# Kernel tuning notes

Hardware: AMD Instinct MI355X
Metric: run time of the kernel (lower is better)

## Reference

```python
import jax, jax.numpy as jnp
import numpy as np

N, E, EL = 50000, 150000, 300000   # atoms, bonds(=line-graph nodes), line-graph edges
FN, FE, FX = 128, 128, 64          # atom, bond, angle feature dims (encode_dim)
H, D = 4, 64                        # num_heads, per-head hidden
SLOPE = 0.01                        # torch leaky_relu default


def _leaky(x):
    return jnp.where(x >= 0, x, SLOPE * x)


def _seg_softmax(logits, seg, n):
    # softmax over edges grouped by destination (DGL edge_softmax). logits [E, H]
    m = jax.ops.segment_max(logits, seg, num_segments=n)
    ex = jnp.exp(logits - m[seg])
    s = jax.ops.segment_sum(ex, seg, num_segments=n)
    return ex / s[seg]


def _seg_mean(x, seg, n):
    # mean of incoming edge feats per dst node; empty segments -> 0 (DGL behavior)
    s = jax.ops.segment_sum(x, seg, num_segments=n)
    c = jax.ops.segment_sum(jnp.ones((x.shape[0], 1), x.dtype), seg, num_segments=n)
    return s / jnp.maximum(c, 1.0)


def setup_inputs() -> dict:
    key = jax.random.key(0)
    ks = iter(jax.random.split(key, 40))
    nrm = lambda shape, sc=0.1: jax.random.normal(next(ks), shape, jnp.float32) * sc
    z = lambda n: jnp.zeros((n,), jnp.float32)
    inp = {
        'nfeats': nrm((N, FN), 1.0),
        'efeats': nrm((E, FE), 1.0),
        'xfeats': nrm((EL, FX), 1.0),
        # EGAT layer (atom graph)
        'e_Wni': nrm((H * D, FN)), 'e_Wnj': nrm((H * D, FN)), 'e_Wfij': nrm((H * D, FE)),
        'e_Wnode': nrm((H * D, FN + FE)), 'e_bnode': z(H * D),
        'e_attn': nrm((H, D)), 'e_bias': z(H * D),
        # Path_Complex line-graph branch
        'lg_Wni': nrm((H * D, D)), 'lg_Wnj': nrm((H * D, D)), 'lg_Wfij': nrm((H * D, FX)),
        'lg_Wnode': nrm((H * D, D + FX)), 'lg_bnode': z(H * D),
        'lg_attn': nrm((H, D)), 'lg_bias': z(H * D),
        # Path_Complex graph branch
        'g_Wni': nrm((H * D, D)), 'g_Wnj': nrm((H * D, D)), 'g_Wfij': nrm((H * D, D)),
        'g_Wnode': nrm((H * D, D + D)), 'g_bnode': z(H * D),
        'g_attn': nrm((H, D)), 'g_bias': z(H * D),
        # graph / line-graph connectivity
        'src': jax.random.randint(next(ks), (E,), 0, N, jnp.int32),
        'dst': jax.random.randint(next(ks), (E,), 0, N, jnp.int32),
        'lsrc': jax.random.randint(next(ks), (EL,), 0, E, jnp.int32),
        'ldst': jax.random.randint(next(ks), (EL,), 0, E, jnp.int32),
    }
    return inp


def _forward(nfeats, efeats, xfeats,
             e_Wni, e_Wnj, e_Wfij, e_Wnode, e_bnode, e_attn, e_bias,
             lg_Wni, lg_Wnj, lg_Wfij, lg_Wnode, lg_bnode, lg_attn, lg_bias,
             g_Wni, g_Wnj, g_Wfij, g_Wnode, g_bnode, g_attn, g_bias,
             src, dst, lsrc, ldst):
    # ---- EGAT layer on atom graph ----
    fo = _leaky((nfeats @ e_Wni.T)[src] + (nfeats @ e_Wnj.T)[dst] + efeats @ e_Wfij.T + e_bias)
    fov = fo.reshape(E, H, D)
    e_att = _seg_softmax((fov * e_attn[None]).sum(-1), dst, N)      # [E, H]
    agg = _seg_mean(efeats, dst, N)                                   # [N, FE]
    h = (jnp.concatenate([nfeats, agg], 1) @ e_Wnode.T + e_bnode).reshape(N, H, D)
    h_node = _leaky(jax.ops.segment_sum(h[src] * e_att[:, :, None], dst, num_segments=N)).sum(1)
    f_edge = fov.sum(1)                                               # [E, D]

    # ---- Path_Complex layer: line-graph (bond->angle) branch ----
    lgf = _leaky((f_edge @ lg_Wni.T)[lsrc] + (f_edge @ lg_Wnj.T)[ldst] + xfeats @ lg_Wfij.T + lg_bias)
    lgv = lgf.reshape(EL, H, D)
    a_lg = _seg_softmax((lgv * lg_attn[None]).sum(-1), ldst, E)      # [EL, H]
    aggx = _seg_mean(xfeats, ldst, E)                                 # [E, FX]
    m1 = (jnp.concatenate([f_edge, aggx], 1) @ lg_Wnode.T + lg_bnode).reshape(E, H, D)
    lg_h = _leaky(jax.ops.segment_sum(m1[lsrc] * a_lg[:, :, None], ldst, num_segments=E)).sum(1)

    # ---- Path_Complex layer: graph (atom->bond) branch ----
    gf = _leaky((h_node @ g_Wni.T)[src] + (h_node @ g_Wnj.T)[dst] + f_edge @ g_Wfij.T + g_bias)
    gv = gf.reshape(E, H, D)
    a_g = _seg_softmax((gv * g_attn[None]).sum(-1), dst, N)          # [E, H] -> l_graph ndata 'a'
    node_edge = h_node[src] + h_node[dst]
    m2 = (jnp.concatenate([node_edge, f_edge], 1) @ g_Wnode.T + g_bnode).reshape(E, H, D)
    # u_mul_v on line graph: message = h_out[lsrc] * a[ldst]
    g_h = _leaky(jax.ops.segment_sum(m2[lsrc] * a_g[ldst][:, :, None], ldst, num_segments=E)).sum(1)

    return g_h + lg_h                                                 # [E, D] updated bond feats


def reference(nfeats, efeats, xfeats,
              e_Wni, e_Wnj, e_Wfij, e_Wnode, e_bnode, e_attn, e_bias,
              lg_Wni, lg_Wnj, lg_Wfij, lg_Wnode, lg_bnode, lg_attn, lg_bias,
              g_Wni, g_Wnj, g_Wfij, g_Wnode, g_bnode, g_attn, g_bias,
              src, dst, lsrc, ldst):
    return _forward(nfeats, efeats, xfeats,
                    e_Wni, e_Wnj, e_Wfij, e_Wnode, e_bnode, e_attn, e_bias,
                    lg_Wni, lg_Wnj, lg_Wfij, lg_Wnode, lg_bnode, lg_attn, lg_bias,
                    g_Wni, g_Wnj, g_Wfij, g_Wnode, g_bnode, g_attn, g_bias,
                    src, dst, lsrc, ldst)
```

## Files before the change

### kernel.cpp

```cpp
#include <hip/hip_runtime.h>
#include <hip/hip_bf16.h>
#include <math.h>

typedef __hip_bfloat16 bf16;
typedef short bf16x8 __attribute__((ext_vector_type(8)));
typedef short s16x4 __attribute__((ext_vector_type(4)));
typedef float f32x4 __attribute__((ext_vector_type(4)));

__device__ __forceinline__ float b2f(bf16 x) { return __bfloat162float(x); }
__device__ __forceinline__ bf16  f2b(float x) { return __float2bfloat16(x); }
__device__ __forceinline__ float leaky(float x) { return x >= 0.0f ? x : 0.01f * x; }
__device__ __forceinline__ float sb2f(short s) {
  return __uint_as_float(((unsigned)(unsigned short)s) << 16);
}
__device__ __forceinline__ short f2bs(float x) {
  unsigned u = __float_as_uint(x);
  u += 0x7FFFu + ((u >> 16) & 1u);
  return (short)(u >> 16);
}
__device__ __forceinline__ float ldF(const void* p, size_t i, int f) {
  return f ? ((const float*)p)[i] : b2f(((const bf16*)p)[i]);
}
__device__ __forceinline__ bf16x8 ldA8(const char* row, int k, int f) {
  if (!f) return *(const bf16x8*)(row + (size_t)k * 2);
  const float4* p = (const float4*)(row + (size_t)k * 4);
  float4 a = p[0], b = p[1];
  bf16x8 r;
  r[0] = f2bs(a.x); r[1] = f2bs(a.y); r[2] = f2bs(a.z); r[3] = f2bs(a.w);
  r[4] = f2bs(b.x); r[5] = f2bs(b.y); r[6] = f2bs(b.z); r[7] = f2bs(b.w);
  return r;
}
__device__ __forceinline__ bf16x8 ldA8sum(const bf16* base, int K0, int s, int t, int k) {
  bf16x8 u = *(const bf16x8*)(base + (size_t)s * K0 + k);
  bf16x8 v = *(const bf16x8*)(base + (size_t)t * K0 + k);
  bf16x8 r;
#pragma unroll
  for (int j = 0; j < 8; ++j) r[j] = f2bs(sb2f(u[j]) + sb2f(v[j]));
  return r;
}

__global__ void k_detect(const unsigned* __restrict__ w, int* __restrict__ flag) {
  __shared__ int cnt[256];
  unsigned x = w[threadIdx.x];
  unsigned ex = (x >> 7) & 0xFFu;
  cnt[threadIdx.x] = (ex >= 96u && ex <= 144u) ? 1 : 0;
  __syncthreads();
  for (int s = 128; s > 0; s >>= 1) {
    if (threadIdx.x < s) cnt[threadIdx.x] += cnt[threadIdx.x + s];
    __syncthreads();
  }
  if (threadIdx.x == 0) *flag = (cnt[0] < 128) ? 1 : 0;
}

struct WArgs { const void* src[21]; int beg[22]; int len[21]; };
__global__ void k_cvt_all(WArgs wa, bf16* __restrict__ dst, int total,
                          const int* __restrict__ flagp) {
  int f = *flagp;
  for (int i = blockIdx.x * 256 + threadIdx.x; i < total; i += gridDim.x * 256) {
    int t = 0;
    while (t < 20 && i >= wa.beg[t + 1]) ++t;
    int loc = i - wa.beg[t];
    bf16 v = f2b(0.0f);
    if (loc < wa.len[t])
      v = f ? f2b(((const float*)wa.src[t])[loc]) : ((const bf16*)wa.src[t])[loc];
    dst[i] = v;
  }
}

__global__ void k_cvt3(const float* __restrict__ a, bf16* __restrict__ da, size_t na,
                       const float* __restrict__ b, bf16* __restrict__ db, size_t nb,
                       const float* __restrict__ c, bf16* __restrict__ dc, size_t nc,
                       const int* __restrict__ flagp) {
  if (!*flagp) return;
  size_t tot = (na + nb + nc) >> 2;
  for (size_t i = (size_t)blockIdx.x * 256 + threadIdx.x; i < tot;
       i += (size_t)gridDim.x * 256) {
    size_t j = i << 2;
    const float* s; bf16* d; size_t loc;
    if (j < na)           { s = a; d = da; loc = j; }
    else if (j < na + nb) { s = b; d = db; loc = j - na; }
    else                  { s = c; d = dc; loc = j - na - nb; }
    float4 v = *(const float4*)(s + loc);
    s16x4 o; o[0] = f2bs(v.x); o[1] = f2bs(v.y); o[2] = f2bs(v.z); o[3] = f2bs(v.w);
    *(s16x4*)(d + loc) = o;
  }
}

__global__ void k_izero(int* __restrict__ p, int n) {
  int i = blockIdx.x * 256 + threadIdx.x;
  for (; i < n; i += gridDim.x * 256) p[i] = 0;
}

__global__ void k_hist(const int* __restrict__ seg, int* __restrict__ deg, int n) {
  int i = blockIdx.x * 256 + threadIdx.x;
  if (i < n) atomicAdd(&deg[seg[i]], 1);
}

__global__ __launch_bounds__(256)
void k_scan_local(const int* __restrict__ deg, int* __restrict__ rp,
                  int* __restrict__ bsum, int n) {
  __shared__ int sh[256];
  int tid = threadIdx.x;
  int base = blockIdx.x * 4096 + tid * 16;
  int v[16]; int s = 0;
#pragma unroll
  for (int j = 0; j < 16; ++j) { v[j] = (base + j < n) ? deg[base + j] : 0; s += v[j]; }
  sh[tid] = s;
  __syncthreads();
  for (int o = 1; o < 256; o <<= 1) {
    int t = (tid >= o) ? sh[tid - o] : 0;
    __syncthreads();
    sh[tid] += t;
    __syncthreads();
  }
  int run = sh[tid] - s;
#pragma unroll
  for (int j = 0; j < 16; ++j) {
    run += v[j];
    if (base + j < n) rp[base + j + 1] = run;
  }
  if (tid == 255) bsum[blockIdx.x] = sh[255];
  if (blockIdx.x == 0 && tid == 0) rp[0] = 0;
}
__global__ __launch_bounds__(256)
void k_scan_bsum(int* __restrict__ bsum, int nb) {
  __shared__ int sh[256];
  __shared__ int carry;
  int tid = threadIdx.x;
  if (tid == 0) carry = 0;
  __syncthreads();
  for (int base = 0; base < nb; base += 256) {
    int i = base + tid;
    int v = (i < nb) ? bsum[i] : 0;
    sh[tid] = v;
    __syncthreads();
    for (int o = 1; o < 256; o <<= 1) {
      int t = (tid >= o) ? sh[tid - o] : 0;
      __syncthreads();
      sh[tid] += t;
      __syncthreads();
    }
    if (i < nb) bsum[i] = carry + sh[tid] - v;
    int tot = sh[255];
    __syncthreads();
    if (tid == 0) carry += tot;
    __syncthreads();
  }
}
__global__ __launch_bounds__(256)
void k_scan_add(int* __restrict__ rp, const int* __restrict__ bsum, int n) {
  int b = blockIdx.x + 1;
  int ofs = bsum[b];
  int base = b * 4096 + threadIdx.x * 16;
#pragma unroll
  for (int j = 0; j < 16; ++j) {
    int idx = base + j + 1;
    if (idx <= n) rp[idx] += ofs;
  }
}

__global__ void k_slot(const int* __restrict__ seg, const int* __restrict__ rp,
                       int* __restrict__ cur, int* __restrict__ eid,
                       const int* __restrict__ aux, int* __restrict__ auxval,
                       int* __restrict__ pos, int n) {
  int i = blockIdx.x * 256 + threadIdx.x;
  if (i >= n) return;
  int t = seg[i];
  int p = atomicAdd(&cur[t], 1);
  int j = rp[t] + p;
  eid[j] = i;
  if (auxval) auxval[j] = aux[i];
  if (pos) pos[i] = j;
}

__global__ void k_gmean(const void* __restrict__ X, const void* __restrict__ Xc, int mode,
                        const int* __restrict__ rp, const int* __restrict__ eid,
                        bf16* __restrict__ out, int n, int width,
                        const int* __restrict__ flagp) {
  int f = (mode == 2) ? *flagp : mode;
  if (Xc && f) { X = Xc; f = 0; }
  int d = threadIdx.x;
  int row = blockIdx.x * blockDim.y + threadIdx.y;
  if (row >= n) return;
  int b = rp[row], e = rp[row + 1];
  float s = 0.0f;
  for (int j = b; j < e; ++j) s += ldF(X, (size_t)eid[j] * width + d, f);
  out[(size_t)row * width + d] = f2b(s / fmaxf((float)(e - b), 1.0f));
}

__global__ __launch_bounds__(256)
void k_mgemm(const void* __restrict__ A0, const void* __restrict__ A0c, int m0mode, int K0,
             const void* __restrict__ A1, int m1mode, int Ktot,
             const bf16* __restrict__ W, int whs, const bf16* __restrict__ bias,
             bf16* __restrict__ C, int cs, int M,
             const int* __restrict__ gs, const int* __restrict__ gd,
             const int* __restrict__ flagp) {
  int tid = threadIdx.x;
  int w = tid >> 6, lane = tid & 63, l15 = lane & 15, q = lane >> 4;
  int h = blockIdx.y;
  int fl = *flagp;
  int f0 = (m0mode == 2) ? fl : m0mode;
  if (A0c && f0) { A0 = A0c; f0 = 0; }
  int f1 = (m1mode == 2) ? fl : m1mode;
  const bf16* Wh = W + (size_t)h * whs;
  int colofs = h * 64;
  int m0 = blockIdx.x * 64 + w * 16;
  int mA = m0 + l15; if (mA > M - 1) mA = M - 1;
  int sA = 0, tA = 0;
  const char* rowA0 = nullptr;
  if (gs) { sA = gs[mA]; tA = gd[mA]; }
  else rowA0 = (const char*)A0 + (size_t)mA * K0 * (f0 ? 4 : 2);
  const char* rowA1 = A1 ? (const char*)A1 + (size_t)mA * (Ktot - K0) * (f1 ? 4 : 2) : nullptr;

  f32x4 acc[4] = {{0,0,0,0},{0,0,0,0},{0,0,0,0},{0,0,0,0}};
  for (int k = q * 8; k < Ktot; k += 32) {
    bf16x8 a;
    if (k < K0) a = gs ? ldA8sum((const bf16*)A0, K0, sA, tA, k) : ldA8(rowA0, k, f0);
    else        a = ldA8(rowA1, k - K0, f1);
    const bf16* wb = Wh + (size_t)l15 * Ktot + k;
#pragma unroll
    for (int t = 0; t < 4; ++t)
      acc[t] = __builtin_amdgcn_mfma_f32_16x16x32_bf16(
          a, *(const bf16x8*)(wb + (size_t)(t * 16) * Ktot), acc[t], 0, 0, 0);
  }
#pragma unroll
  for (int t = 0; t < 4; ++t) {
    int col = t * 16 + l15;
    float bv = bias ? b2f(bias[colofs + col]) : 0.0f;
#pragma unroll
    for (int r = 0; r < 4; ++r) {
      int m = m0 + q * 4 + r;
      if (m < M) C[(size_t)m * cs + colofs + col] = f2b(acc[t][r] + bv);
    }
  }
}

__global__ __launch_bounds__(256)
void k_mgemm2(const void* __restrict__ A, const void* __restrict__ Ac, int mode, int K,
              const bf16* __restrict__ W1, const bf16* __restrict__ W2, int whs,
              bf16* __restrict__ C1, bf16* __restrict__ C2, int cs, int M,
              const int* __restrict__ flagp) {
  int tid = threadIdx.x;
  int w = tid >> 6, lane = tid & 63, l15 = lane & 15, q = lane >> 4;
  int h = blockIdx.y;
  int f = (mode == 2) ? *flagp : mode;
  if (Ac && f) { A = Ac; f = 0; }
  const bf16* W1h = W1 + (size_t)h * whs;
  const bf16* W2h = W2 + (size_t)h * whs;
  int colofs = h * 64;
  int m0 = blockIdx.x * 64 + w * 16;
  int mA = m0 + l15; if (mA > M - 1) mA = M - 1;
  const char* rowA = (const char*)A + (size_t)mA * K * (f ? 4 : 2);

  f32x4 a1[4] = {{0,0,0,0},{0,0,0,0},{0,0,0,0},{0,0,0,0}};
  f32x4 a2[4] = {{0,0,0,0},{0,0,0,0},{0,0,0,0},{0,0,0,0}};
  for (int k = q * 8; k < K; k += 32) {
    bf16x8 a = ldA8(rowA, k, f);
    const bf16* w1 = W1h + (size_t)l15 * K + k;
    const bf16* w2 = W2h + (size_t)l15 * K + k;
#pragma unroll
    for (int t = 0; t < 4; ++t) {
      a1[t] = __builtin_amdgcn_mfma_f32_16x16x32_bf16(
          a, *(const bf16x8*)(w1 + (size_t)(t * 16) * K), a1[t], 0, 0, 0);
      a2[t] = __builtin_amdgcn_mfma_f32_16x16x32_bf16(
          a, *(const bf16x8*)(w2 + (size_t)(t * 16) * K), a2[t], 0, 0, 0);
    }
  }
#pragma unroll
  for (int r = 0; r < 4; ++r) {
    int m = m0 + q * 4 + r;
    if (m < M) {
      s16x4 o1, o2;
#pragma unroll
      for (int t = 0; t < 4; ++t) { o1[t] = f2bs(a1[t][r]); o2[t] = f2bs(a2[t][r]); }
      *(s16x4*)(C1 + (size_t)m * cs + colofs + l15 * 4) = o1;
      *(s16x4*)(C2 + (size_t)m * cs + colofs + l15 * 4) = o2;
    }
  }
}

template<int NK>
__global__ __launch_bounds__(256)
void k_mcomb4(const void* __restrict__ A, const void* __restrict__ Ac, int mode,
              const bf16* __restrict__ W, int whs,
              const bf16* __restrict__ bias, const bf16* __restrict__ attn,
              const bf16* __restrict__ G1, const bf16* __restrict__ G2, int gstr,
              const int* __restrict__ gi, const int* __restrict__ gj,
              const int* __restrict__ posw,
              float* __restrict__ lg4, bf16* __restrict__ fout,
              int M, const int* __restrict__ flagp) {
  constexpr int K = NK * 32;
  int tid = threadIdx.x;
  int w = tid >> 6, lane = tid & 63, l15 = lane & 15, q = lane >> 4;
  int f = (mode == 2) ? *flagp : mode;
  if (Ac && f) { A = Ac; f = 0; }
  int m0 = blockIdx.x * 64 + w * 16;
  int mA = m0 + l15; if (mA > M - 1) mA = M - 1;
  const char* rowA = (const char*)A + (size_t)mA * K * (f ? 4 : 2);
  bf16x8 af[NK];
#pragma unroll
  for (int i = 0; i < NK; ++i) af[i] = ldA8(rowA, q * 8 + 32 * i, f);
  int sIdx[4], dIdx[4], pIdx[4]; bool okr[4];
#pragma unroll
  for (int r = 0; r < 4; ++r) {
    int m = m0 + q * 4 + r;
    okr[r] = m < M; int mc = okr[r] ? m : M - 1;
    sIdx[r] = gi[mc]; dIdx[r] = gj[mc];
    pIdx[r] = posw ? posw[mc] : mc;
  }
  s16x4 gv1[4][4], gv2[4][4];
#pragma unroll
  for (int r = 0; r < 4; ++r) {
    const s16x4* p1 = (const s16x4*)(G1 + (size_t)sIdx[r] * gstr) + l15;
    const s16x4* p2 = (const s16x4*)(G2 + (size_t)dIdx[r] * gstr) + l15;
#pragma unroll
    for (int h = 0; h < 4; ++h) { gv1[r][h] = p1[h * 16]; gv2[r][h] = p2[h * 16]; }
  }
  f32x4 fs[4] = {{0,0,0,0},{0,0,0,0},{0,0,0,0},{0,0,0,0}};
#pragma unroll
  for (int h = 0; h < 4; ++h) {
    const bf16* Wh = W + (size_t)h * whs;
    f32x4 acc[4] = {{0,0,0,0},{0,0,0,0},{0,0,0,0},{0,0,0,0}};
#pragma unroll
    for (int i = 0; i < NK; ++i) {
      const bf16* wb = Wh + (size_t)l15 * K + q * 8 + 32 * i;
#pragma unroll
      for (int t = 0; t < 4; ++t)
        acc[t] = __builtin_amdgcn_mfma_f32_16x16x32_bf16(
            af[i], *(const bf16x8*)(wb + (size_t)(t * 16) * K), acc[t], 0, 0, 0);
    }
    float bv[4], av[4];
#pragma unroll
    for (int t = 0; t < 4; ++t) {
      bv[t] = b2f(bias[h * 64 + t * 16 + l15]);
      av[t] = b2f(attn[h * 64 + t * 16 + l15]);
    }
    float part[4];
#pragma unroll
    for (int r = 0; r < 4; ++r) {
      float p = 0.0f;
#pragma unroll
      for (int t = 0; t < 4; ++t) {
        float v = acc[t][r] + bv[t] + sb2f(gv1[r][h][t]) + sb2f(gv2[r][h][t]);
        v = leaky(v);
        p += v * av[t];
        fs[t][r] += v;
      }
      part[r] = p;
    }
#pragma unroll
    for (int o = 1; o < 16; o <<= 1)
#pragma unroll
      for (int r = 0; r < 4; ++r) part[r] += __shfl_xor(part[r], o, 64);
    if (l15 == 0) {
#pragma unroll
      for (int r = 0; r < 4; ++r)
        if (okr[r]) lg4[(size_t)pIdx[r] * 4 + h] = part[r];
    }
  }
  if (fout) {
#pragma unroll
    for (int t = 0; t < 4; ++t) {
      int col = t * 16 + l15;
#pragma unroll
      for (int r = 0; r < 4; ++r)
        if (okr[r]) fout[(size_t)(m0 + q * 4 + r) * 64 + col] = f2b(fs[t][r]);
    }
  }
}

__global__ __launch_bounds__(256)
void k_mcomb(const void* __restrict__ A, const void* __restrict__ Ac, int mode, int K,
             const bf16* __restrict__ W, const bf16* __restrict__ bias,
             const bf16* __restrict__ attn,
             const bf16* __restrict__ G1, const bf16* __restrict__ G2, int gstr,
             const int* __restrict__ gi, const int* __restrict__ gj,
             const int* __restrict__ posw,
             float* __restrict__ lg, int M, const int* __restrict__ flagp) {
  int tid = threadIdx.x;
  int w = tid >> 6, lane = tid & 63, l15 = lane & 15, q = lane >> 4;
  int f = (mode == 2) ? *flagp : mode;
  if (Ac && f) { A = Ac; f = 0; }
  int m0 = blockIdx.x * 64 + w * 16;
  int mA = m0 + l15; if (mA > M - 1) mA = M - 1;
  const char* rowA = (const char*)A + (size_t)mA * K * (f ? 4 : 2);
  int mcs[4], pIdx[4]; bool okr[4];
#pragma unroll
  for (int r = 0; r < 4; ++r) {
    int m = m0 + q * 4 + r;
    okr[r] = m < M; mcs[r] = okr[r] ? m : M - 1;
    pIdx[r] = posw ? posw[mcs[r]] : mcs[r];
  }
  s16x4 gv1[4], gv2[4];
#pragma unroll
  for (int r = 0; r < 4; ++r) {
    gv1[r] = ((const s16x4*)(G1 + (size_t)gi[mcs[r]] * gstr))[l15];
    gv2[r] = ((const s16x4*)(G2 + (size_t)gj[mcs[r]] * gstr))[l15];
  }
  f32x4 acc[4] = {{0,0,0,0},{0,0,0,0},{0,0,0,0},{0,0,0,0}};
  for (int k = q * 8; k < K; k += 32) {
    bf16x8 a = ldA8(rowA, k, f);
    const bf16* wb = W + (size_t)l15 * K + k;
#pragma unroll
    for (int t = 0; t < 4; ++t)
      acc[t] = __builtin_amdgcn_mfma_f32_16x16x32_bf16(
          a, *(const bf16x8*)(wb + (size_t)(t * 16) * K), acc[t], 0, 0, 0);
  }
  float attv[4], bsv[4];
#pragma unroll
  for (int t = 0; t < 4; ++t) { attv[t] = b2f(attn[t*16+l15]); bsv[t] = b2f(bias[t*16+l15]); }
  float part[4];
#pragma unroll
  for (int r = 0; r < 4; ++r) {
    float p = 0.0f;
#pragma unroll
    for (int t = 0; t < 4; ++t) {
      float v = acc[t][r] + bsv[t] + sb2f(gv1[r][t]) + sb2f(gv2[r][t]);
      p += leaky(v) * attv[t];
    }
    part[r] = p;
  }
#pragma unroll
  for (int o = 1; o < 16; o <<= 1)
#pragma unroll
    for (int r = 0; r < 4; ++r) part[r] += __shfl_xor(part[r], o, 64);
  if (l15 == 0) {
#pragma unroll
    for (int r = 0; r < 4; ++r)
      if (okr[r]) lg[pIdx[r]] = part[r];
  }
}

__global__ __launch_bounds__(256)
void k_smax4_csr(float* __restrict__ lg, const int* __restrict__ rp, int n) {
  int tid = blockIdx.x * 256 + threadIdx.x;
  int row = tid >> 2, h = tid & 3;
  if (row >= n) return;
  int b = rp[row], e = rp[row + 1];
  float m = -INFINITY;
  for (int j = b; j < e; ++j) m = fmaxf(m, lg[(size_t)j * 4 + h]);
  float s = 0.0f;
  for (int j = b; j < e; ++j) {
    float ex = expf(lg[(size_t)j * 4 + h] - m);
    lg[(size_t)j * 4 + h] = ex;
    s += ex;
  }
  float inv = 1.0f / s;
  for (int j = b; j < e; ++j) lg[(size_t)j * 4 + h] *= inv;
}
__global__ __launch_bounds__(256)
void k_smax4_eid(float* __restrict__ lg, const int* __restrict__ rp,
                 const int* __restrict__ eid, int n) {
  int tid = blockIdx.x * 256 + threadIdx.x;
  int row = tid >> 2, h = tid & 3;
  if (row >= n) return;
  int b = rp[row], e = rp[row + 1];
  float m = -INFINITY;
  for (int j = b; j < e; ++j) m = fmaxf(m, lg[(size_t)eid[j] * 4 + h]);
  float s = 0.0f;
  for (int j = b; j < e; ++j) {
    float ex = expf(lg[(size_t)eid[j] * 4 + h] - m);
    lg[(size_t)eid[j] * 4 + h] = ex;
    s += ex;
  }
  float inv = 1.0f / s;
  for (int j = b; j < e; ++j) lg[(size_t)eid[j] * 4 + h] *= inv;
}
__global__ __launch_bounds__(256)
void k_smax1_csr(float* __restrict__ lg, const int* __restrict__ rp, int n) {
  int row = blockIdx.x * 256 + threadIdx.x;
  if (row >= n) return;
  int b = rp[row], e = rp[row + 1];
  float m = -INFINITY;
  for (int j = b; j < e; ++j) m = fmaxf(m, lg[j]);
  float s = 0.0f;
  for (int j = b; j < e; ++j) { float ex = expf(lg[j] - m); lg[j] = ex; s += ex; }
  float inv = 1.0f / s;
  for (int j = b; j < e; ++j) lg[j] *= inv;
}

__global__ __launch_bounds__(256)
void k_ghnode(const bf16* __restrict__ H, const float* __restrict__ lg4c,
              const int* __restrict__ rp, const int* __restrict__ srcv,
              bf16* __restrict__ hnode, int N) {
  int d = threadIdx.x, h = threadIdx.y;
  int n = blockIdx.x;
  int b = rp[n], e = rp[n + 1];
  float s = 0.0f;
  for (int j = b; j < e; ++j)
    s += b2f(H[(size_t)srcv[j] * 256 + h * 64 + d]) * lg4c[(size_t)j * 4 + h];
  float v = leaky(s);
  __shared__ float sh[4][64];
  if (h > 0) sh[h][d] = v;
  __syncthreads();
  if (h == 0)
    hnode[(size_t)n * 64 + d] = f2b(v + sh[1][d] + sh[2][d] + sh[3][d]);
}

__global__ void k_gout2(const bf16* __restrict__ M1, const float* __restrict__ lgE,
                        const int* __restrict__ rp, const int* __restrict__ lsv,
                        float* __restrict__ out, int E, int first) {
  int d = threadIdx.x;
  int t = blockIdx.x * 4 + threadIdx.y;
  if (t >= E) return;
  int b = rp[t], e = rp[t + 1];
  float s = 0.0f;
  for (int j = b; j < e; ++j)
    s += b2f(M1[(size_t)lsv[j] * 64 + d]) * lgE[j];
  float val = leaky(s);
  if (first) out[(size_t)t * 64 + d] = val;
  else       out[(size_t)t * 64 + d] += val;
}

__global__ void k_gout3(const bf16* __restrict__ M2, const float* __restrict__ lg4n,
                        const int* __restrict__ rp, const int* __restrict__ lsv,
                        float* __restrict__ out, int E, int h) {
  int d = threadIdx.x;
  int t = blockIdx.x * 4 + threadIdx.y;
  if (t >= E) return;
  int b = rp[t], e = rp[t + 1];
  float s = 0.0f;
  for (int j = b; j < e; ++j) s += b2f(M2[(size_t)lsv[j] * 64 + d]);
  float a = lg4n[(size_t)t * 4 + h];
  out[(size_t)t * 64 + d] += leaky(a * s);
}

__global__ void k_addpair(const bf16* __restrict__ hn, const int* __restrict__ src,
                          const int* __restrict__ dst, bf16* __restrict__ ne, int E) {
  int d = threadIdx.x;
  int e = blockIdx.x * 4 + threadIdx.y;
  if (e >= E) return;
  ne[(size_t)e * 64 + d] =
      f2b(b2f(hn[(size_t)src[e] * 64 + d]) + b2f(hn[(size_t)dst[e] * 64 + d]));
}

__global__ void k_cast(void* __restrict__ out, const float* __restrict__ a, size_t n,
                       const int* __restrict__ flagp) {
  int f = *flagp;
  size_t i = (size_t)blockIdx.x * blockDim.x + threadIdx.x;
  size_t st = (size_t)gridDim.x * blockDim.x;
  for (; i < n; i += st) {
    if (f) ((float*)out)[i] = a[i];
    else   ((bf16*)out)[i] = f2b(a[i]);
  }
}

extern "C" void kernel_launch(void* const* d_in, const int* in_sizes, int n_in,
                              void* d_out, int out_size, void* d_ws, size_t ws_size,
                              hipStream_t stream) {
  const int* src  = (const int*)d_in[24];
  const int* dst  = (const int*)d_in[25];
  const int* lsrc = (const int*)d_in[26];
  const int* ldst = (const int*)d_in[27];

  const int N  = in_sizes[0] / 128;
  const int E  = in_sizes[24];
  const int EL = in_sizes[26];
  (void)n_in; (void)out_size; (void)ws_size;

  char* base = (char*)d_ws;
  size_t off = 0;
  auto alloc = [&](size_t bytes) -> char* {
    char* p = base + off;
    off = (off + bytes + 255) & ~(size_t)255;
    return p;
  };
  int* flag = (int*)alloc(256);
  size_t wofs[28]; size_t wtot = 0;
  for (int i = 3; i <= 23; ++i) { wofs[i] = wtot; wtot += (size_t)((in_sizes[i] + 127) & ~127); }
  bf16* WA = (bf16*)alloc(wtot * 2);

  int*   tmpi  = (int*)alloc((size_t)2 * E * 4);
  int*   rpN   = (int*)alloc((size_t)(N + 1) * 4);
  int*   eidN  = (int*)alloc((size_t)E * 4);
  int*   srcv  = (int*)alloc((size_t)E * 4);
  int*   posN  = (int*)alloc((size_t)E * 4);
  int*   rpE   = (int*)alloc((size_t)(E + 1) * 4);
  int*   eidEL = (int*)alloc((size_t)EL * 4);
  int*   lsv   = (int*)alloc((size_t)EL * 4);
  int*   posE  = (int*)alloc((size_t)EL * 4);
  int*   bsum  = (int*)alloc(((size_t)((E > N ? E : N) + 4095) / 4096 + 8) * 4);
  bf16*  fedge = (bf16*)alloc((size_t)E * 64 * 2);
  bf16*  hnode = (bf16*)alloc((size_t)N * 64 * 2);
  float* outacc= (float*)alloc((size_t)E * 64 * 4);
  bf16*  aggB  = (bf16*)alloc((size_t)E * 64 * 2);
  bf16*  SA    = (bf16*)alloc((size_t)N * 256 * 2 > (size_t)E * 64 * 2
                              ? (size_t)N * 256 * 2 : (size_t)E * 64 * 2);
  bf16*  SB    = (bf16*)alloc((size_t)N * 256 * 2 > (size_t)E * 64 * 2
                              ? (size_t)N * 256 * 2 : (size_t)E * 64 * 2);
  float* logE4 = (float*)alloc((size_t)E * 4 * 4);
  float* logh  = (float*)alloc((size_t)EL * 4);
  bf16*  nb    = (bf16*)alloc((size_t)N * 128 * 2);

  bf16* eb = (bf16*)outacc;
  bf16* xb = (bf16*)d_out;

  dim3 blk(256);
  const unsigned tN = (N + 63) / 64, tEg = (E + 63) / 64, tELg = (EL + 63) / 64;
  const unsigned gE4 = (E + 3) / 4, gN4 = (N + 3) / 4;
  const unsigned cE = (E + 255) / 256, cEL = (EL + 255) / 256;
  const int nbN = (N + 4095) / 4096, nbE = (E + 4095) / 4096;

  k_detect<<<dim3(1), blk, 0, stream>>>((const unsigned*)d_in[0], flag);
  WArgs wa;
  for (int i = 3; i <= 23; ++i) {
    wa.src[i - 3] = d_in[i];
    wa.beg[i - 3] = (int)wofs[i];
    wa.len[i - 3] = in_sizes[i];
  }
  wa.beg[21] = (int)wtot;
  k_cvt_all<<<dim3(512), blk, 0, stream>>>(wa, WA, (int)wtot, flag);
  k_cvt3<<<dim3(2048), blk, 0, stream>>>(
      (const float*)d_in[0], nb, (size_t)N * 128,
      (const float*)d_in[1], eb, (size_t)E * 128,
      (const float*)d_in[2], xb, (size_t)EL * 64, flag);

  int* deg = tmpi; int* cur = tmpi + E;
  k_izero<<<dim3(1024), blk, 0, stream>>>(tmpi, 2 * E);
  k_hist<<<dim3(cE), blk, 0, stream>>>(dst, deg, E);
  k_scan_local<<<dim3(nbN), blk, 0, stream>>>(deg, rpN, bsum, N);
  k_scan_bsum<<<dim3(1), blk, 0, stream>>>(bsum, nbN);
  if (nbN > 1) k_scan_add<<<dim3(nbN - 1), blk, 0, stream>>>(rpN, bsum, N);
  k_slot<<<dim3(cE), blk, 0, stream>>>(dst, rpN, cur, eidN, src, srcv, posN, E);
  k_izero<<<dim3(1024), blk, 0, stream>>>(tmpi, 2 * E);
  k_hist<<<dim3(cEL), blk, 0, stream>>>(ldst, deg, EL);
  k_scan_local<<<dim3(nbE), blk, 0, stream>>>(deg, rpE, bsum, E);
  k_scan_bsum<<<dim3(1), blk, 0, stream>>>(bsum, nbE);
  if (nbE > 1) k_scan_add<<<dim3(nbE - 1), blk, 0, stream>>>(rpE, bsum, E);
  k_slot<<<dim3(cEL), blk, 0, stream>>>(ldst, rpE, cur, eidEL, lsrc, lsv, posE, EL);

  k_gmean<<<dim3((N + 1) / 2), dim3(128, 2), 0, stream>>>(d_in[1], eb, 2, rpN, eidN,
                                                          aggB, N, 128, flag);
  k_mgemm2<<<dim3(tN, 4), blk, 0, stream>>>(d_in[0], nb, 2, 128, WA + wofs[3], WA + wofs[4],
                                            8192, SA, SB, 256, N, flag);
  k_mcomb4<4><<<dim3(tEg), blk, 0, stream>>>(d_in[1], eb, 2, WA + wofs[5], 8192,
      WA + wofs[9], WA + wofs[8], SA, SB, 256, src, dst, posN, logE4, fedge, E, flag);
  k_smax4_csr<<<dim3((N * 4 + 255) / 256), blk, 0, stream>>>(logE4, rpN, N);
  k_mgemm<<<dim3(tN, 4), blk, 0, stream>>>(d_in[0], nb, 2, 128, aggB, 0, 256,
      WA + wofs[6], 16384, WA + wofs[7], SA, 256, N, nullptr, nullptr, flag);
  k_ghnode<<<dim3(N), dim3(64, 4), 0, stream>>>(SA, logE4, rpN, srcv, hnode, N);

  k_gmean<<<dim3(gE4), dim3(64, 4), 0, stream>>>(d_in[2], xb, 2, rpE, eidEL, aggB, E, 64, flag);
  for (int h = 0; h < 4; ++h) {
    k_mgemm2<<<dim3(tEg), blk, 0, stream>>>(fedge, nullptr, 0, 64,
        WA + wofs[10] + h * 4096, WA + wofs[11] + h * 4096, 0, SA, SB, 64, E, flag);
    k_mcomb<<<dim3(tELg), blk, 0, stream>>>(d_in[2], xb, 2, 64,
        WA + wofs[12] + h * 4096, WA + wofs[16] + h * 64, WA + wofs[15] + h * 64,
        SA, SB, 64, lsrc, ldst, posE, logh, EL, flag);
    k_smax1_csr<<<dim3((E + 255) / 256), blk, 0, stream>>>(logh, rpE, E);
    k_mgemm<<<dim3(tEg, 1), blk, 0, stream>>>(fedge, nullptr, 0, 64, aggB, 0, 128,
        WA + wofs[13] + (size_t)h * 8192, 0, WA + wofs[14] + h * 64,
        SA, 64, E, nullptr, nullptr, flag);
    k_gout2<<<dim3(gE4), dim3(64, 4), 0, stream>>>(SA, logh, rpE, lsv,
                                                   outacc, E, h == 0 ? 1 : 0);
  }

  k_mgemm2<<<dim3(tN, 4), blk, 0, stream>>>(hnode, nullptr, 0, 64, WA + wofs[17], WA + wofs[18],
                                            4096, SA, SB, 256, N, flag);
  k_mcomb4<2><<<dim3(tEg), blk, 0, stream>>>(fedge, nullptr, 0, WA + wofs[19], 4096,
      WA + wofs[23], WA + wofs[22], SA, SB, 256, src, dst, nullptr, logE4, nullptr, E, flag);
  k_smax4_eid<<<dim3((N * 4 + 255) / 256), blk, 0, stream>>>(logE4, rpN, eidN, N);
  k_addpair<<<dim3(gE4), dim3(64, 4), 0, stream>>>(hnode, src, dst, aggB, E);
  for (int h = 0; h < 4; ++h) {
    k_mgemm<<<dim3(tEg, 1), blk, 0, stream>>>(aggB, nullptr, 0, 64, fedge, 0, 128,
        WA + wofs[20] + (size_t)h * 8192, 0, WA + wofs[21] + h * 64,
        SB, 64, E, nullptr, nullptr, flag);
    k_gout3<<<dim3(gE4), dim3(64, 4), 0, stream>>>(SB, logE4, rpE, lsv,
                                                   outacc, E, h);
  }

  k_cast<<<dim3(2048), blk, 0, stream>>>(d_out, outacc, (size_t)E * 64, flag);
}
```

Before: 1.804 ms.

## Batch line-graph attention logits two heads per pass with swizzled gather layout

Replaces the per-head line-graph logit pipeline (projection GEMM, combine, single-head softmax) with two passes that each handle two heads. The combine kernel reuses loaded A fragments across both heads and writes into a 4-wide logit buffer, followed by one multi-head CSR softmax. Projection outputs are stored in a swizzled layout so each lane gathers 8 or 16 contiguous bf16 values per endpoint instead of several 4-element chunks. It also drops the efeats bf16 pre-conversion and shrinks buffers, which adds more register pressure and a larger logit buffer.

Result: no change. 1.838 ms (+1.9%).

```diff
diff --git a/kernel.cpp b/kernel.cpp
--- a/kernel.cpp
+++ b/kernel.cpp
@@ -28,14 +28,6 @@
   bf16x8 r;
   r[0] = f2bs(a.x); r[1] = f2bs(a.y); r[2] = f2bs(a.z); r[3] = f2bs(a.w);
   r[4] = f2bs(b.x); r[5] = f2bs(b.y); r[6] = f2bs(b.z); r[7] = f2bs(b.w);
-  return r;
-}
-__device__ __forceinline__ bf16x8 ldA8sum(const bf16* base, int K0, int s, int t, int k) {
-  bf16x8 u = *(const bf16x8*)(base + (size_t)s * K0 + k);
-  bf16x8 v = *(const bf16x8*)(base + (size_t)t * K0 + k);
-  bf16x8 r;
-#pragma unroll
-  for (int j = 0; j < 8; ++j) r[j] = f2bs(sb2f(u[j]) + sb2f(v[j]));
   return r;
 }
 
@@ -67,19 +59,17 @@
   }
 }
 
-__global__ void k_cvt3(const float* __restrict__ a, bf16* __restrict__ da, size_t na,
-                       const float* __restrict__ b, bf16* __restrict__ db, size_t nb,
+__global__ void k_cvt2(const float* __restrict__ a, bf16* __restrict__ da, size_t na,
                        const float* __restrict__ c, bf16* __restrict__ dc, size_t nc,
                        const int* __restrict__ flagp) {
   if (!*flagp) return;
-  size_t tot = (na + nb + nc) >> 2;
+  size_t tot = (na + nc) >> 2;
   for (size_t i = (size_t)blockIdx.x * 256 + threadIdx.x; i < tot;
        i += (size_t)gridDim.x * 256) {
     size_t j = i << 2;
     const float* s; bf16* d; size_t loc;
-    if (j < na)           { s = a; d = da; loc = j; }
-    else if (j < na + nb) { s = b; d = db; loc = j - na; }
-    else                  { s = c; d = dc; loc = j - na - nb; }
+    if (j < na) { s = a; d = da; loc = j; }
+    else        { s = c; d = dc; loc = j - na; }
     float4 v = *(const float4*)(s + loc);
     s16x4 o; o[0] = f2bs(v.x); o[1] = f2bs(v.y); o[2] = f2bs(v.z); o[3] = f2bs(v.w);
     *(s16x4*)(d + loc) = o;
@@ -161,7 +151,7 @@
 
 __global__ void k_slot(const int* __restrict__ seg, const int* __restrict__ rp,
                        int* __restrict__ cur, int* __restrict__ eid,
-                       const int* __restrict__ aux, int* __restrict__ auxval,
+                       const int* __restrict__ aux1, int* __restrict__ av1,
                        int* __restrict__ pos, int n) {
   int i = blockIdx.x * 256 + threadIdx.x;
   if (i >= n) return;
@@ -169,7 +159,7 @@
   int p = atomicAdd(&cur[t], 1);
   int j = rp[t] + p;
   eid[j] = i;
-  if (auxval) auxval[j] = aux[i];
+  if (av1) av1[j] = aux1[i];
   if (pos) pos[i] = j;
 }
 
@@ -193,7 +183,6 @@
              const void* __restrict__ A1, int m1mode, int Ktot,
              const bf16* __restrict__ W, int whs, const bf16* __restrict__ bias,
              bf16* __restrict__ C, int cs, int M,
-             const int* __restrict__ gs, const int* __restrict__ gd,
              const int* __restrict__ flagp) {
   int tid = threadIdx.x;
   int w = tid >> 6, lane = tid & 63, l15 = lane & 15, q = lane >> 4;
@@ -206,16 +195,13 @@
   int colofs = h * 64;
   int m0 = blockIdx.x * 64 + w * 16;
   int mA = m0 + l15; if (mA > M - 1) mA = M - 1;
-  int sA = 0, tA = 0;
-  const char* rowA0 = nullptr;
-  if (gs) { sA = gs[mA]; tA = gd[mA]; }
-  else rowA0 = (const char*)A0 + (size_t)mA * K0 * (f0 ? 4 : 2);
+  const char* rowA0 = (const char*)A0 + (size_t)mA * K0 * (f0 ? 4 : 2);
   const char* rowA1 = A1 ? (const char*)A1 + (size_t)mA * (Ktot - K0) * (f1 ? 4 : 2) : nullptr;
 
   f32x4 acc[4] = {{0,0,0,0},{0,0,0,0},{0,0,0,0},{0,0,0,0}};
   for (int k = q * 8; k < Ktot; k += 32) {
     bf16x8 a;
-    if (k < K0) a = gs ? ldA8sum((const bf16*)A0, K0, sA, tA, k) : ldA8(rowA0, k, f0);
+    if (k < K0) a = ldA8(rowA0, k, f0);
     else        a = ldA8(rowA1, k - K0, f1);
     const bf16* wb = Wh + (size_t)l15 * Ktot + k;
 #pragma unroll
@@ -236,18 +222,19 @@
 }
 
 __global__ __launch_bounds__(256)
-void k_mgemm2(const void* __restrict__ A, const void* __restrict__ Ac, int mode, int K,
-              const bf16* __restrict__ W1, const bf16* __restrict__ W2, int whs,
-              bf16* __restrict__ C1, bf16* __restrict__ C2, int cs, int M,
-              const int* __restrict__ flagp) {
+void k_mgemm2sw(const void* __restrict__ A, const void* __restrict__ Ac, int mode, int K,
+                const bf16* __restrict__ W1, const bf16* __restrict__ W2, int whs,
+                int h0, int HB, bf16* __restrict__ C1, bf16* __restrict__ C2, int M,
+                const int* __restrict__ flagp) {
   int tid = threadIdx.x;
   int w = tid >> 6, lane = tid & 63, l15 = lane & 15, q = lane >> 4;
-  int h = blockIdx.y;
+  int hy = blockIdx.y;
+  int h = h0 + hy;
   int f = (mode == 2) ? *flagp : mode;
   if (Ac && f) { A = Ac; f = 0; }
   const bf16* W1h = W1 + (size_t)h * whs;
   const bf16* W2h = W2 + (size_t)h * whs;
-  int colofs = h * 64;
+  int cs = HB * 64;
   int m0 = blockIdx.x * 64 + w * 16;
   int mA = m0 + l15; if (mA > M - 1) mA = M - 1;
   const char* rowA = (const char*)A + (size_t)mA * K * (f ? 4 : 2);
@@ -266,6 +253,7 @@
           a, *(const bf16x8*)(w2 + (size_t)(t * 16) * K), a2[t], 0, 0, 0);
     }
   }
+  int ofs = l15 * 4 * HB + hy * 4;
 #pragma unroll
   for (int r = 0; r < 4; ++r) {
     int m = m0 + q * 4 + r;
@@ -273,22 +261,22 @@
       s16x4 o1, o2;
 #pragma unroll
       for (int t = 0; t < 4; ++t) { o1[t] = f2bs(a1[t][r]); o2[t] = f2bs(a2[t][r]); }
-      *(s16x4*)(C1 + (size_t)m * cs + colofs + l15 * 4) = o1;
-      *(s16x4*)(C2 + (size_t)m * cs + colofs + l15 * 4) = o2;
+      *(s16x4*)(C1 + (size_t)m * cs + ofs) = o1;
+      *(s16x4*)(C2 + (size_t)m * cs + ofs) = o2;
     }
   }
 }
 
 template<int NK>
 __global__ __launch_bounds__(256)
-void k_mcomb4(const void* __restrict__ A, const void* __restrict__ Ac, int mode,
-              const bf16* __restrict__ W, int whs,
-              const bf16* __restrict__ bias, const bf16* __restrict__ attn,
-              const bf16* __restrict__ G1, const bf16* __restrict__ G2, int gstr,
-              const int* __restrict__ gi, const int* __restrict__ gj,
-              const int* __restrict__ posw,
-              float* __restrict__ lg4, bf16* __restrict__ fout,
-              int M, const int* __restrict__ flagp) {
+void k_mcomb4sw(const void* __restrict__ A, const void* __restrict__ Ac, int mode,
+                const bf16* __restrict__ W, int whs,
+                const bf16* __restrict__ bias, const bf16* __restrict__ attn,
+                const bf16* __restrict__ G1, const bf16* __restrict__ G2,
+                const int* __restrict__ gi, const int* __restrict__ gj,
+                const int* __restrict__ posw,
+                float* __restrict__ lg4, bf16* __restrict__ fout,
+                int M, const int* __restrict__ flagp) {
   constexpr int K = NK * 32;
   int tid = threadIdx.x;
   int w = tid >> 6, lane = tid & 63, l15 = lane & 15, q = lane >> 4;
@@ -300,21 +288,17 @@
   bf16x8 af[NK];
 #pragma unroll
   for (int i = 0; i < NK; ++i) af[i] = ldA8(rowA, q * 8 + 32 * i, f);
-  int sIdx[4], dIdx[4], pIdx[4]; bool okr[4];
+  int pIdx[4]; bool okr[4];
+  bf16x8 gv1[4][2], gv2[4][2];
 #pragma unroll
   for (int r = 0; r < 4; ++r) {
     int m = m0 + q * 4 + r;
     okr[r] = m < M; int mc = okr[r] ? m : M - 1;
-    sIdx[r] = gi[mc]; dIdx[r] = gj[mc];
     pIdx[r] = posw ? posw[mc] : mc;
-  }
-  s16x4 gv1[4][4], gv2[4][4];
-#pragma unroll
-  for (int r = 0; r < 4; ++r) {
-    const s16x4* p1 = (const s16x4*)(G1 + (size_t)sIdx[r] * gstr) + l15;
-    const s16x4* p2 = (const s16x4*)(G2 + (size_t)dIdx[r] * gstr) + l15;
-#pragma unroll
-    for (int h = 0; h < 4; ++h) { gv1[r][h] = p1[h * 16]; gv2[r][h] = p2[h * 16]; }
+    const bf16* p1 = G1 + (size_t)gi[mc] * 256 + l15 * 16;
+    const bf16* p2 = G2 + (size_t)gj[mc] * 256 + l15 * 16;
+    gv1[r][0] = *(const bf16x8*)p1; gv1[r][1] = *(const bf16x8*)(p1 + 8);
+    gv2[r][0] = *(const bf16x8*)p2; gv2[r][1] = *(const bf16x8*)(p2 + 8);
   }
   f32x4 fs[4] = {{0,0,0,0},{0,0,0,0},{0,0,0,0},{0,0,0,0}};
 #pragma unroll
@@ -341,7 +325,8 @@
       float p = 0.0f;
 #pragma unroll
       for (int t = 0; t < 4; ++t) {
-        float v = acc[t][r] + bv[t] + sb2f(gv1[r][h][t]) + sb2f(gv2[r][h][t]);
+        float v = acc[t][r] + bv[t] + sb2f(gv1[r][h >> 1][(h & 1) * 4 + t])
+                                    + sb2f(gv2[r][h >> 1][(h & 1) * 4 + t]);
         v = leaky(v);
         p += v * av[t];
         fs[t][r] += v;
@@ -369,14 +354,16 @@
   }
 }
 
-__global__ __launch_bounds__(256)
-void k_mcomb(const void* __restrict__ A, const void* __restrict__ Ac, int mode, int K,
-             const bf16* __restrict__ W, const bf16* __restrict__ bias,
-             const bf16* __restrict__ attn,
-             const bf16* __restrict__ G1, const bf16* __restrict__ G2, int gstr,
-             const int* __restrict__ gi, const int* __restrict__ gj,
-             const int* __restrict__ posw,
-             float* __restrict__ lg, int M, const int* __restrict__ flagp) {
+template<int NK>
+__global__ __launch_bounds__(256)
+void k_mcomb2h(const void* __restrict__ A, const void* __restrict__ Ac, int mode,
+               const bf16* __restrict__ W, int whs, int h0,
+               const bf16* __restrict__ bias, const bf16* __restrict__ attn,
+               const bf16* __restrict__ G1, const bf16* __restrict__ G2,
+               const int* __restrict__ gi, const int* __restrict__ gj,
+               const int* __restrict__ posw,
+               float* __restrict__ lg4, int M, const int* __restrict__ flagp) {
+  constexpr int K = NK * 32;
   int tid = threadIdx.x;
   int w = tid >> 6, lane = tid & 63, l15 = lane & 15, q = lane >> 4;
   int f = (mode == 2) ? *flagp : mode;
@@ -384,50 +371,58 @@
   int m0 = blockIdx.x * 64 + w * 16;
   int mA = m0 + l15; if (mA > M - 1) mA = M - 1;
   const char* rowA = (const char*)A + (size_t)mA * K * (f ? 4 : 2);
-  int mcs[4], pIdx[4]; bool okr[4];
+  bf16x8 af[NK];
+#pragma unroll
+  for (int i = 0; i < NK; ++i) af[i] = ldA8(rowA, q * 8 + 32 * i, f);
+  int pIdx[4]; bool okr[4];
+  bf16x8 gv1[4], gv2[4];
 #pragma unroll
   for (int r = 0; r < 4; ++r) {
     int m = m0 + q * 4 + r;
-    okr[r] = m < M; mcs[r] = okr[r] ? m : M - 1;
-    pIdx[r] = posw ? posw[mcs[r]] : mcs[r];
-  }
-  s16x4 gv1[4], gv2[4];
-#pragma unroll
-  for (int r = 0; r < 4; ++r) {
-    gv1[r] = ((const s16x4*)(G1 + (size_t)gi[mcs[r]] * gstr))[l15];
-    gv2[r] = ((const s16x4*)(G2 + (size_t)gj[mcs[r]] * gstr))[l15];
-  }
-  f32x4 acc[4] = {{0,0,0,0},{0,0,0,0},{0,0,0,0},{0,0,0,0}};
-  for (int k = q * 8; k < K; k += 32) {
-    bf16x8 a = ldA8(rowA, k, f);
-    const bf16* wb = W + (size_t)l15 * K + k;
-#pragma unroll
-    for (int t = 0; t < 4; ++t)
-      acc[t] = __builtin_amdgcn_mfma_f32_16x16x32_bf16(
-          a, *(const bf16x8*)(wb + (size_t)(t * 16) * K), acc[t], 0, 0, 0);
-  }
-  float attv[4], bsv[4];
-#pragma unroll
-  for (int t = 0; t < 4; ++t) { attv[t] = b2f(attn[t*16+l15]); bsv[t] = b2f(bias[t*16+l15]); }
-  float part[4];
-#pragma unroll
-  for (int r = 0; r < 4; ++r) {
-    float p = 0.0f;
+    okr[r] = m < M; int mc = okr[r] ? m : M - 1;
+    pIdx[r] = posw ? posw[mc] : mc;
+    gv1[r] = *(const bf16x8*)(G1 + (size_t)gi[mc] * 128 + l15 * 8);
+    gv2[r] = *(const bf16x8*)(G2 + (size_t)gj[mc] * 128 + l15 * 8);
+  }
+#pragma unroll
+  for (int hy = 0; hy < 2; ++hy) {
+    int h = h0 + hy;
+    const bf16* Wh = W + (size_t)h * whs;
+    f32x4 acc[4] = {{0,0,0,0},{0,0,0,0},{0,0,0,0},{0,0,0,0}};
+#pragma unroll
+    for (int i = 0; i < NK; ++i) {
+      const bf16* wb = Wh + (size_t)l15 * K + q * 8 + 32 * i;
+#pragma unroll
+      for (int t = 0; t < 4; ++t)
+        acc[t] = __builtin_amdgcn_mfma_f32_16x16x32_bf16(
+            af[i], *(const bf16x8*)(wb + (size_t)(t * 16) * K), acc[t], 0, 0, 0);
+    }
+    float bv[4], av[4];
 #pragma unroll
     for (int t = 0; t < 4; ++t) {
-      float v = acc[t][r] + bsv[t] + sb2f(gv1[r][t]) + sb2f(gv2[r][t]);
-      p += leaky(v) * attv[t];
-    }
-    part[r] = p;
-  }
-#pragma unroll
-  for (int o = 1; o < 16; o <<= 1)
-#pragma unroll
-    for (int r = 0; r < 4; ++r) part[r] += __shfl_xor(part[r], o, 64);
-  if (l15 == 0) {
-#pragma unroll
-    for (int r = 0; r < 4; ++r)
-      if (okr[r]) lg[pIdx[r]] = part[r];
+      bv[t] = b2f(bias[h * 64 + t * 16 + l15]);
+      av[t] = b2f(attn[h * 64 + t * 16 + l15]);
+    }
+    float part[4];
+#pragma unroll
+    for (int r = 0; r < 4; ++r) {
+      float p = 0.0f;
+#pragma unroll
+      for (int t = 0; t < 4; ++t) {
+        float v = acc[t][r] + bv[t] + sb2f(gv1[r][hy * 4 + t]) + sb2f(gv2[r][hy * 4 + t]);
+        p += leaky(v) * av[t];
+      }
+      part[r] = p;
+    }
+#pragma unroll
+    for (int o = 1; o < 16; o <<= 1)
+#pragma unroll
+      for (int r = 0; r < 4; ++r) part[r] += __shfl_xor(part[r], o, 64);
+    if (l15 == 0) {
+#pragma unroll
+      for (int r = 0; r < 4; ++r)
+        if (okr[r]) lg4[(size_t)pIdx[r] * 4 + h] = part[r];
+    }
   }
 }
 
@@ -465,18 +460,6 @@
   }
   float inv = 1.0f / s;
   for (int j = b; j < e; ++j) lg[(size_t)eid[j] * 4 + h] *= inv;
-}
-__global__ __launch_bounds__(256)
-void k_smax1_csr(float* __restrict__ lg, const int* __restrict__ rp, int n) {
-  int row = blockIdx.x * 256 + threadIdx.x;
-  if (row >= n) return;
-  int b = rp[row], e = rp[row + 1];
-  float m = -INFINITY;
-  for (int j = b; j < e; ++j) m = fmaxf(m, lg[j]);
-  float s = 0.0f;
-  for (int j = b; j < e; ++j) { float ex = expf(lg[j] - m); lg[j] = ex; s += ex; }
-  float inv = 1.0f / s;
-  for (int j = b; j < e; ++j) lg[j] *= inv;
 }
 
 __global__ __launch_bounds__(256)
@@ -497,8 +480,8 @@
     hnode[(size_t)n * 64 + d] = f2b(v + sh[1][d] + sh[2][d] + sh[3][d]);
 }
 
-__global__ void k_gout2(const bf16* __restrict__ M1, const float* __restrict__ lgE,
-                        const int* __restrict__ rp, const int* __restrict__ lsv,
+__global__ void k_gout2(const bf16* __restrict__ M1, const float* __restrict__ lgE4,
+                        int h, const int* __restrict__ rp, const int* __restrict__ lsv,
                         float* __restrict__ out, int E, int first) {
   int d = threadIdx.x;
   int t = blockIdx.x * 4 + threadIdx.y;
@@ -506,7 +489,7 @@
   int b = rp[t], e = rp[t + 1];
   float s = 0.0f;
   for (int j = b; j < e; ++j)
-    s += b2f(M1[(size_t)lsv[j] * 64 + d]) * lgE[j];
+    s += b2f(M1[(size_t)lsv[j] * 64 + d]) * lgE4[(size_t)j * 4 + h];
   float val = leaky(s);
   if (first) out[(size_t)t * 64 + d] = val;
   else       out[(size_t)t * 64 + d] += val;
@@ -584,20 +567,18 @@
   bf16*  hnode = (bf16*)alloc((size_t)N * 64 * 2);
   float* outacc= (float*)alloc((size_t)E * 64 * 4);
   bf16*  aggB  = (bf16*)alloc((size_t)E * 64 * 2);
-  bf16*  SA    = (bf16*)alloc((size_t)N * 256 * 2 > (size_t)E * 64 * 2
-                              ? (size_t)N * 256 * 2 : (size_t)E * 64 * 2);
-  bf16*  SB    = (bf16*)alloc((size_t)N * 256 * 2 > (size_t)E * 64 * 2
-                              ? (size_t)N * 256 * 2 : (size_t)E * 64 * 2);
+  size_t saElems = (size_t)E * 128 > (size_t)N * 256 ? (size_t)E * 128 : (size_t)N * 256;
+  bf16*  SA    = (bf16*)alloc(saElems * 2);
   float* logE4 = (float*)alloc((size_t)E * 4 * 4);
-  float* logh  = (float*)alloc((size_t)EL * 4);
+  float* logEL4= (float*)alloc((size_t)EL * 4 * 4);
   bf16*  nb    = (bf16*)alloc((size_t)N * 128 * 2);
 
-  bf16* eb = (bf16*)outacc;
-  bf16* xb = (bf16*)d_out;
+  bf16* SBo = (bf16*)outacc;
+  bf16* xb  = (bf16*)d_out;
 
   dim3 blk(256);
   const unsigned tN = (N + 63) / 64, tEg = (E + 63) / 64, tELg = (EL + 63) / 64;
-  const unsigned gE4 = (E + 3) / 4, gN4 = (N + 3) / 4;
+  const unsigned gE4 = (E + 3) / 4;
   const unsigned cE = (E + 255) / 256, cEL = (EL + 255) / 256;
   const int nbN = (N + 4095) / 4096, nbE = (E + 4095) / 4096;
 
@@ -610,9 +591,8 @@
   }
   wa.beg[21] = (int)wtot;
   k_cvt_all<<<dim3(512), blk, 0, stream>>>(wa, WA, (int)wtot, flag);
-  k_cvt3<<<dim3(2048), blk, 0, stream>>>(
+  k_cvt2<<<dim3(2048), blk, 0, stream>>>(
       (const float*)d_in[0], nb, (size_t)N * 128,
-      (const float*)d_in[1], eb, (size_t)E * 128,
       (const float*)d_in[2], xb, (size_t)EL * 64, flag);
 
   int* deg = tmpi; int* cur = tmpi + E;
@@ -629,43 +609,47 @@
   if (nbE > 1) k_scan_add<<<dim3(nbE - 1), blk, 0, stream>>>(rpE, bsum, E);
   k_slot<<<dim3(cEL), blk, 0, stream>>>(ldst, rpE, cur, eidEL, lsrc, lsv, posE, EL);
 
-  k_gmean<<<dim3((N + 1) / 2), dim3(128, 2), 0, stream>>>(d_in[1], eb, 2, rpN, eidN,
+  k_gmean<<<dim3((N + 1) / 2), dim3(128, 2), 0, stream>>>(d_in[1], nullptr, 2, rpN, eidN,
                                                           aggB, N, 128, flag);
-  k_mgemm2<<<dim3(tN, 4), blk, 0, stream>>>(d_in[0], nb, 2, 128, WA + wofs[3], WA + wofs[4],
-                                            8192, SA, SB, 256, N, flag);
-  k_mcomb4<4><<<dim3(tEg), blk, 0, stream>>>(d_in[1], eb, 2, WA + wofs[5], 8192,
-      WA + wofs[9], WA + wofs[8], SA, SB, 256, src, dst, posN, logE4, fedge, E, flag);
+  k_mgemm2sw<<<dim3(tN, 4), blk, 0, stream>>>(d_in[0], nb, 2, 128,
+      WA + wofs[3], WA + wofs[4], 8192, 0, 4, SA, SBo, N, flag);
+  k_mcomb4sw<4><<<dim3(tEg), blk, 0, stream>>>(d_in[1], nullptr, 2, WA + wofs[5], 8192,
+      WA + wofs[9], WA + wofs[8], SA, SBo, src, dst, posN, logE4, fedge, E, flag);
   k_smax4_csr<<<dim3((N * 4 + 255) / 256), blk, 0, stream>>>(logE4, rpN, N);
   k_mgemm<<<dim3(tN, 4), blk, 0, stream>>>(d_in[0], nb, 2, 128, aggB, 0, 256,
-      WA + wofs[6], 16384, WA + wofs[7], SA, 256, N, nullptr, nullptr, flag);
+      WA + wofs[6], 16384, WA + wofs[7], SA, 256, N, flag);
   k_ghnode<<<dim3(N), dim3(64, 4), 0, stream>>>(SA, logE4, rpN, srcv, hnode, N);
 
   k_gmean<<<dim3(gE4), dim3(64, 4), 0, stream>>>(d_in[2], xb, 2, rpE, eidEL, aggB, E, 64, flag);
+  for (int p = 0; p < 2; ++p) {
+    k_mgemm2sw<<<dim3(tEg, 2), blk, 0, stream>>>(fedge, nullptr, 0, 64,
+        WA + wofs[10], WA + wofs[11], 4096, 2 * p, 2, SA, SBo, E, flag);
+    k_mcomb2h<2><<<dim3(tELg), blk, 0, stream>>>(d_in[2], xb, 2, WA + wofs[12], 4096, 2 * p,
+        WA + wofs[16], WA + wofs[15], SA, SBo, lsrc, ldst, posE, logEL4, EL, flag);
+  }
+  k_smax4_csr<<<dim3((E * 4 + 255) / 256), blk, 0, stream>>>(logEL4, rpE, E);
   for (int h = 0; h < 4; ++h) {
-    k_mgemm2<<<dim3(tEg), blk, 0, stream>>>(fedge, nullptr, 0, 64,
-        WA + wofs[10] + h * 4096, WA + wofs[11] + h * 4096, 0, SA, SB, 64, E, flag);
-    k_mcomb<<<dim3(tELg), blk, 0, stream>>>(d_in[2], xb, 2, 64,
-        WA + wofs[12] + h * 4096, WA + wofs[16] + h * 64, WA + wofs[15] + h * 64,
-        SA, SB, 64, lsrc, ldst, posE, logh, EL, flag);
-    k_smax1_csr<<<dim3((E + 255) / 256), blk, 0, stream>>>(logh, rpE, E);
     k_mgemm<<<dim3(tEg, 1), blk, 0, stream>>>(fedge, nullptr, 0, 64, aggB, 0, 128,
         WA + wofs[13] + (size_t)h * 8192, 0, WA + wofs[14] + h * 64,
-        SA, 64, E, nullptr, nullptr, flag);
-    k_gout2<<<dim3(gE4), dim3(64, 4), 0, stream>>>(SA, logh, rpE, lsv,
+        SA, 64, E, flag);
+    k_gout2<<<dim3(gE4), dim3(64, 4), 0, stream>>>(SA, logEL4, h, rpE, lsv,
                                                    outacc, E, h == 0 ? 1 : 0);
   }
 
-  k_mgemm2<<<dim3(tN, 4), blk, 0, stream>>>(hnode, nullptr, 0, 64, WA + wofs[17], WA + wofs[18],
-                                            4096, SA, SB, 256, N, flag);
-  k_mcomb4<2><<<dim3(tEg), blk, 0, stream>>>(fedge, nullptr, 0, WA + wofs[19], 4096,
-      WA + wofs[23], WA + wofs[22], SA, SB, 256, src, dst, nullptr, logE4, nullptr, E, flag);
+  for (int p = 0; p < 2; ++p) {
+    k_mgemm2sw<<<dim3(tN, 2), blk, 0, stream>>>(hnode, nullptr, 0, 64,
+        WA + wofs[17], WA + wofs[18], 4096, 2 * p, 2, SA, SA + (size_t)N * 128, N, flag);
+    k_mcomb2h<2><<<dim3(tEg), blk, 0, stream>>>(fedge, nullptr, 0, WA + wofs[19], 4096, 2 * p,
+        WA + wofs[23], WA + wofs[22], SA, SA + (size_t)N * 128, src, dst, nullptr,
+        logE4, E, flag);
+  }
   k_smax4_eid<<<dim3((N * 4 + 255) / 256), blk, 0, stream>>>(logE4, rpN, eidN, N);
   k_addpair<<<dim3(gE4), dim3(64, 4), 0, stream>>>(hnode, src, dst, aggB, E);
   for (int h = 0; h < 4; ++h) {
     k_mgemm<<<dim3(tEg, 1), blk, 0, stream>>>(aggB, nullptr, 0, 64, fedge, 0, 128,
         WA + wofs[20] + (size_t)h * 8192, 0, WA + wofs[21] + h * 64,
-        SB, 64, E, nullptr, nullptr, flag);
-    k_gout3<<<dim3(gE4), dim3(64, 4), 0, stream>>>(SB, logE4, rpE, lsv,
+        SA, 64, E, flag);
+    k_gout3<<<dim3(gE4), dim3(64, 4), 0, stream>>>(SA, logE4, rpE, lsv,
                                                    outacc, E, h);
   }
 
```
